# Performance work log

Hardware: AMD Instinct MI355X
Metric: run time of the kernel (lower is better)

## Reference

```python
import jax, jax.numpy as jnp
import numpy as np

# Binary (sign) weight linear: y = x @ sign(W)^T + b

def _binarize(w):
    # sign with sign(0) mapped to +1, as in typical BinaryLinear impls
    return jnp.where(w >= 0, 1.0, -1.0).astype(w.dtype)

def setup_inputs() -> dict:
    key = jax.random.key(0)
    ks = jax.random.split(key, 7)
    B = 65536
    x = jax.random.normal(ks[0], (B, 28, 28), dtype=jnp.float32)
    W1 = jax.random.normal(ks[1], (1000, 784), dtype=jnp.float32) * 0.05
    b1 = jax.random.normal(ks[2], (1000,), dtype=jnp.float32) * 0.01
    W2 = jax.random.normal(ks[3], (500, 1000), dtype=jnp.float32) * 0.05
    b2 = jax.random.normal(ks[4], (500,), dtype=jnp.float32) * 0.01
    W3 = jax.random.normal(ks[5], (10, 500), dtype=jnp.float32) * 0.05
    b3 = jax.random.normal(ks[6], (10,), dtype=jnp.float32) * 0.01
    return {"x": x, "W1": W1, "b1": b1, "W2": W2, "b2": b2, "W3": W3, "b3": b3}

def reference(x, W1, b1, W2, b2, W3, b3):
    h = x.reshape(x.shape[0], -1)                      # [B, 784]
    h = jnp.maximum(h @ _binarize(W1).T + b1, 0.0)     # [B, 1000]
    h = jnp.maximum(h @ _binarize(W2).T + b2, 0.0)     # [B, 500]
    return h @ _binarize(W3).T + b3                    # [B, 10]
```

## Files before the change

### kernel.cpp

```cpp
#include <hip/hip_runtime.h>
#include <stdint.h>


typedef __attribute__((ext_vector_type(8))) short bf16x8;
typedef __attribute__((ext_vector_type(4))) float f32x4;

typedef const __attribute__((address_space(1))) unsigned int* as1_u32p;
typedef __attribute__((address_space(3))) unsigned int* as3_u32p;

__device__ __forceinline__ void glds16(const void* g, void* l) {
  __builtin_amdgcn_global_load_lds((as1_u32p)g, (as3_u32p)l, 16, 0, 0);
}

__device__ __forceinline__ unsigned short f2bf(float f) {
  union { float f; unsigned u; } c;
  c.f = f;
  unsigned u = c.u;
  u += 0x7FFFu + ((u >> 16) & 1u);
  return (unsigned short)(u >> 16);
}

__global__ void binarize_kernel(const float* __restrict__ src, int Ns, int Ks,
                                short* __restrict__ dst, int Np, int Kp) {
  int idx = blockIdx.x * 256 + threadIdx.x;
  if (idx >= Np * Kp) return;
  int n = idx / Kp;
  int k = idx - n * Kp;
  short v = 0;
  if (n < Ns && k < Ks)
    v = (src[n * Ks + k] >= 0.0f) ? (short)0x3F80 : (short)0xBF80;
  dst[idx] = v;
}

__global__ void convert_x_kernel(const float* __restrict__ X, short* __restrict__ Xp) {
  const int g = blockIdx.x * 256 + threadIdx.x;
  if (g >= 65536 * 104) return;
  const int row = g / 104;
  const int c = (g - row * 104) * 8;
  short tmp[8];
  if (c < 784) {
    const float* s = X + (size_t)row * 784 + c;
    float4 f0 = *(const float4*)s;
    float4 f1 = *(const float4*)(s + 4);
    tmp[0] = (short)f2bf(f0.x); tmp[1] = (short)f2bf(f0.y);
    tmp[2] = (short)f2bf(f0.z); tmp[3] = (short)f2bf(f0.w);
    tmp[4] = (short)f2bf(f1.x); tmp[5] = (short)f2bf(f1.y);
    tmp[6] = (short)f2bf(f1.z); tmp[7] = (short)f2bf(f1.w);
  } else {
#pragma unroll
    for (int i = 0; i < 8; ++i) tmp[i] = 0;
  }
  *(bf16x8*)(Xp + (size_t)row * 832 + c) = *(bf16x8*)(tmp);
}

template <int KP, int NIT, int NP, int NR, int GLOG>
__global__ __launch_bounds__(256, 2)
void gemm_bk64(const short* __restrict__ A, const short* __restrict__ Wb,
               const float* __restrict__ bias, short* __restrict__ Hout) {
  __shared__ short As0[128 * 32];
  __shared__ short As1[128 * 32];
  __shared__ short Bs0[128 * 32];
  __shared__ short Bs1[128 * 32];

  const int d = blockIdx.x;
  const int xcd = d & 7;
  const int slot = d >> 3;
  const int j = slot & ((1 << GLOG) - 1);
  const int m0 = ((xcd << 6) + (slot >> GLOG)) * 128;
  const int n0 = j * 128;
  const int start = (j * NIT) >> GLOG;

  const int tid = threadIdx.x;
  const int lane = tid & 63;
  const int wave = tid >> 6;
  const int wm = wave >> 1, wn = wave & 1;
  const int l15 = lane & 15;
  const int quad = lane >> 4;

  const int sr = wave * 16 + (lane >> 2);
  const int sks = (lane & 3) * 8;
  const short* asrc = A + (size_t)(m0 + sr) * KP + sks;
  const short* bsrc = Wb + (size_t)(n0 + sr) * KP + sks;
  const int sdst = (wave * 16) * 32;

  f32x4 acc[4][4];
#pragma unroll
  for (int i = 0; i < 4; ++i)
#pragma unroll
    for (int j2 = 0; j2 < 4; ++j2) acc[i][j2] = (f32x4){0.f, 0.f, 0.f, 0.f};

  for (int it = 0; it < NIT; ++it) {
    int kit = start + it;
    if (kit >= NIT) kit -= NIT;
    const int k0 = kit * 64;

    glds16(asrc + k0, As0 + sdst);
    glds16(asrc + k0 + (size_t)64 * KP, As0 + sdst + 64 * 32);
    glds16(asrc + k0 + 32, As1 + sdst);
    glds16(asrc + k0 + 32 + (size_t)64 * KP, As1 + sdst + 64 * 32);
    glds16(bsrc + k0, Bs0 + sdst);
    glds16(bsrc + k0 + (size_t)64 * KP, Bs0 + sdst + 64 * 32);
    glds16(bsrc + k0 + 32, Bs1 + sdst);
    glds16(bsrc + k0 + 32 + (size_t)64 * KP, Bs1 + sdst + 64 * 32);
    __syncthreads();

#pragma unroll
    for (int h = 0; h < 2; ++h) {
      const short* As = h ? As1 : Bs0 - 128 * 32;
      const short* ab = (h ? As1 : As0) + (wm * 64 + l15) * 32 + quad * 8;
      const short* bb = (h ? Bs1 : Bs0) + (wn * 64 + l15) * 32 + quad * 8;
      bf16x8 af[4], bfr[4];
#pragma unroll
      for (int i = 0; i < 4; ++i) af[i] = *(const bf16x8*)(ab + i * 16 * 32);
#pragma unroll
      for (int j2 = 0; j2 < 4; ++j2) bfr[j2] = *(const bf16x8*)(bb + j2 * 16 * 32);
#pragma unroll
      for (int i = 0; i < 4; ++i)
#pragma unroll
        for (int j2 = 0; j2 < 4; ++j2)
          acc[i][j2] = __builtin_amdgcn_mfma_f32_16x16x32_bf16(af[i], bfr[j2], acc[i][j2], 0, 0, 0);
    }
    __syncthreads();
  }

#pragma unroll
  for (int j2 = 0; j2 < 4; ++j2) {
    const int n = n0 + wn * 64 + j2 * 16 + l15;
    const float bv = (n < NR) ? bias[n] : 0.f;
#pragma unroll
    for (int i = 0; i < 4; ++i) {
      const int mr = m0 + wm * 64 + i * 16 + quad * 4;
#pragma unroll
      for (int r = 0; r < 4; ++r) {
        float v = acc[i][j2][r] + bv;
        v = v > 0.f ? v : 0.f;
        Hout[(size_t)(mr + r) * NP + n] = (short)f2bf(v);
      }
    }
  }
}

__global__ __launch_bounds__(256, 2)
void gemm1_fused_kernel(const float* __restrict__ X, const short* __restrict__ Wb,
                        const float* __restrict__ bias, short* __restrict__ H) {
  constexpr int K = 784, KP = 832, NP = 1024, NR = 1000;
  __shared__ short As[128 * 32];
  __shared__ short Bs[128 * 32];

  const int tid = threadIdx.x;
  const int lane = tid & 63;
  const int wave = tid >> 6;
  const int wm = wave >> 1, wn = wave & 1;
  const int l15 = lane & 15;
  const int quad = lane >> 4;
  const int m0 = blockIdx.y * 128;
  const int n0 = blockIdx.x * 128;

  const int ar = tid >> 1;
  const int aks = (tid & 1) * 16;
  const float* xrow = X + (size_t)(m0 + ar) * K;
  short* adst = As + ar * 32 + aks;

  const int br = wave * 16 + (lane >> 2);
  const int bks = (lane & 3) * 8;
  const short* brow0 = Wb + (size_t)(n0 + br) * KP + bks;
  short* bdst = Bs + (wave * 16) * 32;

  f32x4 acc[4][4];
#pragma unroll
  for (int i = 0; i < 4; ++i)
#pragma unroll
    for (int j2 = 0; j2 < 4; ++j2) acc[i][j2] = (f32x4){0.f, 0.f, 0.f, 0.f};

  for (int k0 = 0; k0 < KP; k0 += 32) {
    glds16(brow0 + k0, bdst);
    glds16(brow0 + k0 + (size_t)64 * KP, bdst + 64 * 32);
    short tmp[16];
#pragma unroll
    for (int c = 0; c < 4; ++c) {
      const int kk = k0 + aks + c * 4;
      float4 f;
      if (kk + 3 < K)
        f = *(const float4*)(xrow + kk);
      else
        f = make_float4(0.f, 0.f, 0.f, 0.f);
      tmp[c * 4 + 0] = (short)f2bf(f.x);
      tmp[c * 4 + 1] = (short)f2bf(f.y);
      tmp[c * 4 + 2] = (short)f2bf(f.z);
      tmp[c * 4 + 3] = (short)f2bf(f.w);
    }
    *(bf16x8*)(adst) = *(bf16x8*)(tmp);
    *(bf16x8*)(adst + 8) = *(bf16x8*)(tmp + 8);
    __syncthreads();

    const short* abase = As + (size_t)(wm * 64 + l15) * 32 + quad * 8;
    const short* bbase = Bs + (size_t)(wn * 64 + l15) * 32 + quad * 8;
    bf16x8 af[4], bfr[4];
#pragma unroll
    for (int i = 0; i < 4; ++i) af[i] = *(const bf16x8*)(abase + i * 16 * 32);
#pragma unroll
    for (int j2 = 0; j2 < 4; ++j2) bfr[j2] = *(const bf16x8*)(bbase + j2 * 16 * 32);
#pragma unroll
    for (int i = 0; i < 4; ++i)
#pragma unroll
      for (int j2 = 0; j2 < 4; ++j2)
        acc[i][j2] = __builtin_amdgcn_mfma_f32_16x16x32_bf16(af[i], bfr[j2], acc[i][j2], 0, 0, 0);
    __syncthreads();
  }

#pragma unroll
  for (int j2 = 0; j2 < 4; ++j2) {
    const int n = n0 + wn * 64 + j2 * 16 + l15;
    const float bv = (n < NR) ? bias[n] : 0.f;
#pragma unroll
    for (int i = 0; i < 4; ++i) {
      const int mr = m0 + wm * 64 + i * 16 + quad * 4;
#pragma unroll
      for (int r = 0; r < 4; ++r) {
        float v = acc[i][j2][r] + bv;
        v = v > 0.f ? v : 0.f;
        H[(size_t)(mr + r) * NP + n] = (short)f2bf(v);
      }
    }
  }
}

__global__ __launch_bounds__(256, 2)
void gemm3_kernel(const short* __restrict__ Hin, const short* __restrict__ Wb,
                  const float* __restrict__ bias, float* __restrict__ Out) {
  constexpr int KP = 512;
  __shared__ short As[64 * KP];

  const int tid = threadIdx.x;
  const int lane = tid & 63;
  const int wave = tid >> 6;
  const int l15 = lane & 15;
  const int quad = lane >> 4;
  const int m0 = blockIdx.x * 64;

  bf16x8 bw[16];
#pragma unroll
  for (int kk = 0; kk < 16; ++kk)
    bw[kk] = *(const bf16x8*)(Wb + l15 * KP + kk * 32 + quad * 8);

  const short* asrc = Hin + (size_t)(m0 + wave * 16) * KP + lane * 8;
  short* adst = As + (size_t)(wave * 16) * KP;
#pragma unroll
  for (int t = 0; t < 16; ++t)
    glds16(asrc + (size_t)t * KP, adst + (size_t)t * KP);

  __syncthreads();

  f32x4 acc = (f32x4){0.f, 0.f, 0.f, 0.f};
  const short* abase = As + (size_t)(wave * 16 + l15) * KP + quad * 8;
#pragma unroll
  for (int kk = 0; kk < 16; ++kk) {
    bf16x8 af = *(const bf16x8*)(abase + kk * 32);
    acc = __builtin_amdgcn_mfma_f32_16x16x32_bf16(af, bw[kk], acc, 0, 0, 0);
  }

  if (l15 < 10) {
    const float bv = bias[l15];
#pragma unroll
    for (int r = 0; r < 4; ++r) {
      const int mr = m0 + wave * 16 + quad * 4 + r;
      Out[(size_t)mr * 10 + l15] = acc[r] + bv;
    }
  }
}

extern "C" void kernel_launch(void* const* d_in, const int* in_sizes, int n_in,
                              void* d_out, int out_size, void* d_ws, size_t ws_size,
                              hipStream_t stream) {
  const float* x = (const float*)d_in[0];
  const float* W1 = (const float*)d_in[1];
  const float* b1 = (const float*)d_in[2];
  const float* W2 = (const float*)d_in[3];
  const float* b2 = (const float*)d_in[4];
  const float* W3 = (const float*)d_in[5];
  const float* b3 = (const float*)d_in[6];
  float* out = (float*)d_out;

  const size_t szW1 = (size_t)1024 * 832 * 2;
  const size_t szW2 = (size_t)512 * 1024 * 2;
  const size_t szW3 = (size_t)16 * 512 * 2;
  const size_t szH1 = (size_t)65536 * 1024 * 2;
  const size_t szXp = (size_t)65536 * 832 * 2;
  const size_t need = szW1 + szW2 + szW3 + szH1 + szXp;

  uint8_t* p = (uint8_t*)d_ws;
  short* W1b = (short*)p; p += szW1;
  short* W2b = (short*)p; p += szW2;
  short* W3b = (short*)p; p += szW3;
  short* h1 = (short*)p; p += szH1;
  short* Z = (short*)p;

  binarize_kernel<<<(1024 * 832 + 255) / 256, 256, 0, stream>>>(W1, 1000, 784, W1b, 1024, 832);
  binarize_kernel<<<(512 * 1024 + 255) / 256, 256, 0, stream>>>(W2, 500, 1000, W2b, 512, 1024);
  binarize_kernel<<<(16 * 512 + 255) / 256, 256, 0, stream>>>(W3, 10, 500, W3b, 16, 512);

  if (ws_size >= need) {
    short* Xp = Z;
    short* h2 = Z;
    convert_x_kernel<<<(65536 * 104 + 255) / 256, 256, 0, stream>>>(x, Xp);
    gemm_bk64<832, 13, 1024, 1000, 3><<<4096, 256, 0, stream>>>(Xp, W1b, b1, h1);
    gemm_bk64<1024, 16, 512, 500, 2><<<2048, 256, 0, stream>>>(h1, W2b, b2, h2);
    gemm3_kernel<<<1024, 256, 0, stream>>>(h2, W3b, b3, out);
  } else {
    short* h2 = Z;
    gemm1_fused_kernel<<<dim3(8, 512), 256, 0, stream>>>(x, W1b, b1, h1);
    gemm_bk64<1024, 16, 512, 500, 2><<<2048, 256, 0, stream>>>(h1, W2b, b2, h2);
    gemm3_kernel<<<1024, 256, 0, stream>>>(h2, W3b, b3, out);
  }
}
```

Measured before the change: 575.2 us.

## Replace 128x128 GEMM with double-buffered 256x256 tile kernel using swizzled LDS

Replaces the 128x128, 256-thread GEMM for layers 1 and 2 with a 256x256, 512-thread kernel. The new kernel double-buffers LDS, prefetching two K-tiles ahead, and splits each K-step so that MFMA work overlaps the next global-to-LDS loads. It uses an XOR-swizzled LDS layout to avoid bank conflicts and raises wave priority around the MFMA blocks. The larger tile cuts global traffic per flop, in exchange for more LDS (128KB per block) and more accumulator registers, which may reduce occupancy.

```diff
diff --git a/kernel.cpp b/kernel.cpp
--- a/kernel.cpp
+++ b/kernel.cpp
@@ -53,86 +53,139 @@
   *(bf16x8*)(Xp + (size_t)row * 832 + c) = *(bf16x8*)(tmp);
 }
 
-template <int KP, int NIT, int NP, int NR, int GLOG>
-__global__ __launch_bounds__(256, 2)
-void gemm_bk64(const short* __restrict__ A, const short* __restrict__ Wb,
-               const float* __restrict__ bias, short* __restrict__ Hout) {
-  __shared__ short As0[128 * 32];
-  __shared__ short As1[128 * 32];
-  __shared__ short Bs0[128 * 32];
-  __shared__ short Bs1[128 * 32];
-
+template <int KP, int NKT, int NP, int NR, int NT>
+__global__ __launch_bounds__(512, 2)
+void gemm256(const short* __restrict__ A, const short* __restrict__ Wb,
+             const float* __restrict__ bias, short* __restrict__ Hout) {
+  __shared__ short Asm[2][256 * 64];
+  __shared__ short Bsm[2][256 * 64];
+
+  constexpr int NWG8 = (256 * NT) >> 3;
   const int d = blockIdx.x;
-  const int xcd = d & 7;
-  const int slot = d >> 3;
-  const int j = slot & ((1 << GLOG) - 1);
-  const int m0 = ((xcd << 6) + (slot >> GLOG)) * 128;
-  const int n0 = j * 128;
-  const int start = (j * NIT) >> GLOG;
+  const int lid = (d & 7) * NWG8 + (d >> 3);
+  const int mi = lid / NT;
+  const int ni = lid - mi * NT;
+  const int m0 = mi << 8;
+  const int n0 = ni << 8;
+  const int start = (ni * NKT) / NT;
 
   const int tid = threadIdx.x;
   const int lane = tid & 63;
-  const int wave = tid >> 6;
-  const int wm = wave >> 1, wn = wave & 1;
+  const int w = tid >> 6;
+  const int wm = w >> 2;
+  const int wn = w & 3;
   const int l15 = lane & 15;
   const int quad = lane >> 4;
 
-  const int sr = wave * 16 + (lane >> 2);
-  const int sks = (lane & 3) * 8;
-  const short* asrc = A + (size_t)(m0 + sr) * KP + sks;
-  const short* bsrc = Wb + (size_t)(n0 + sr) * KP + sks;
-  const int sdst = (wave * 16) * 32;
-
-  f32x4 acc[4][4];
-#pragma unroll
-  for (int i = 0; i < 4; ++i)
-#pragma unroll
-    for (int j2 = 0; j2 < 4; ++j2) acc[i][j2] = (f32x4){0.f, 0.f, 0.f, 0.f};
-
-  for (int it = 0; it < NIT; ++it) {
-    int kit = start + it;
-    if (kit >= NIT) kit -= NIT;
-    const int k0 = kit * 64;
-
-    glds16(asrc + k0, As0 + sdst);
-    glds16(asrc + k0 + (size_t)64 * KP, As0 + sdst + 64 * 32);
-    glds16(asrc + k0 + 32, As1 + sdst);
-    glds16(asrc + k0 + 32 + (size_t)64 * KP, As1 + sdst + 64 * 32);
-    glds16(bsrc + k0, Bs0 + sdst);
-    glds16(bsrc + k0 + (size_t)64 * KP, Bs0 + sdst + 64 * 32);
-    glds16(bsrc + k0 + 32, Bs1 + sdst);
-    glds16(bsrc + k0 + 32 + (size_t)64 * KP, Bs1 + sdst + 64 * 32);
-    __syncthreads();
-
-#pragma unroll
-    for (int h = 0; h < 2; ++h) {
-      const short* As = h ? As1 : Bs0 - 128 * 32;
-      const short* ab = (h ? As1 : As0) + (wm * 64 + l15) * 32 + quad * 8;
-      const short* bb = (h ? Bs1 : Bs0) + (wn * 64 + l15) * 32 + quad * 8;
-      bf16x8 af[4], bfr[4];
-#pragma unroll
-      for (int i = 0; i < 4; ++i) af[i] = *(const bf16x8*)(ab + i * 16 * 32);
-#pragma unroll
-      for (int j2 = 0; j2 < 4; ++j2) bfr[j2] = *(const bf16x8*)(bb + j2 * 16 * 32);
-#pragma unroll
-      for (int i = 0; i < 4; ++i)
-#pragma unroll
-        for (int j2 = 0; j2 < 4; ++j2)
-          acc[i][j2] = __builtin_amdgcn_mfma_f32_16x16x32_bf16(af[i], bfr[j2], acc[i][j2], 0, 0, 0);
-    }
-    __syncthreads();
-  }
-
-#pragma unroll
-  for (int j2 = 0; j2 < 4; ++j2) {
-    const int n = n0 + wn * 64 + j2 * 16 + l15;
+  const int srow = (w << 3) + (lane >> 3);
+  const int scol = ((lane & 7) ^ (lane >> 3)) << 3;
+  const short* ag = A + (size_t)(m0 + srow) * KP + scol;
+  const short* bg = Wb + (size_t)(n0 + srow) * KP + scol;
+  short* const la = &Asm[0][0] + (w << 9);
+  short* const lb = &Bsm[0][0] + (w << 9);
+
+  auto stageA = [&](int pb, int kit) {
+    const short* s = ag + kit * 64;
+    short* dst = la + (pb << 14);
+    glds16(s, dst);
+    glds16(s + (size_t)64 * KP, dst + 4096);
+    glds16(s + (size_t)128 * KP, dst + 8192);
+    glds16(s + (size_t)192 * KP, dst + 12288);
+  };
+  auto stageB = [&](int pb, int kit) {
+    const short* s = bg + kit * 64;
+    short* dst = lb + (pb << 14);
+    glds16(s, dst);
+    glds16(s + (size_t)64 * KP, dst + 4096);
+    glds16(s + (size_t)128 * KP, dst + 8192);
+    glds16(s + (size_t)192 * KP, dst + 12288);
+  };
+
+  const int arow = ((wm << 7) + l15) << 6;
+  const int brow = ((wn << 6) + l15) << 6;
+  const int sl0 = (quad ^ (lane & 7)) << 3;
+  const int sl1 = sl0 ^ 32;
+
+  f32x4 acc[8][4];
+#pragma unroll
+  for (int i = 0; i < 8; ++i)
+#pragma unroll
+    for (int j = 0; j < 4; ++j) acc[i][j] = (f32x4){0.f, 0.f, 0.f, 0.f};
+
+  int k1 = start + 1; if (k1 >= NKT) k1 -= NKT;
+  stageA(0, start); stageB(0, start);
+  stageA(1, k1);    stageB(1, k1);
+  asm volatile("s_waitcnt vmcnt(8)" ::: "memory");
+  __builtin_amdgcn_s_barrier();
+
+  for (int it = 0; it < NKT; ++it) {
+    const int pb = it & 1;
+    const short* Ab = &Asm[pb][0];
+    const short* Bb = &Bsm[pb][0];
+
+    bf16x8 a0[8], b0[4], a1[8], b1[4];
+#pragma unroll
+    for (int i = 0; i < 8; ++i) a0[i] = *(const bf16x8*)(Ab + arow + i * 1024 + sl0);
+#pragma unroll
+    for (int j = 0; j < 4; ++j) b0[j] = *(const bf16x8*)(Bb + brow + j * 1024 + sl0);
+    __builtin_amdgcn_s_barrier();
+    __builtin_amdgcn_s_setprio(1);
+#pragma unroll
+    for (int i = 0; i < 4; ++i)
+#pragma unroll
+      for (int j = 0; j < 4; ++j)
+        acc[i][j] = __builtin_amdgcn_mfma_f32_16x16x32_bf16(a0[i], b0[j], acc[i][j], 0, 0, 0);
+    __builtin_amdgcn_s_setprio(0);
+
+    #pragma unroll
+    for (int i = 0; i < 8; ++i) a1[i] = *(const bf16x8*)(Ab + arow + i * 1024 + sl1);
+#pragma unroll
+    for (int j = 0; j < 4; ++j) b1[j] = *(const bf16x8*)(Bb + brow + j * 1024 + sl1);
+    __builtin_amdgcn_s_barrier();
+    asm volatile("s_waitcnt lgkmcnt(0)" ::: "memory");
+    __builtin_amdgcn_s_setprio(1);
+#pragma unroll
+    for (int i = 4; i < 8; ++i)
+#pragma unroll
+      for (int j = 0; j < 4; ++j)
+        acc[i][j] = __builtin_amdgcn_mfma_f32_16x16x32_bf16(a0[i], b0[j], acc[i][j], 0, 0, 0);
+    __builtin_amdgcn_s_setprio(0);
+    __builtin_amdgcn_s_barrier();
+
+    const int it2 = it + 2;
+    int kit2 = start + it2; if (kit2 >= NKT) kit2 -= NKT;
+    const bool stg = (it2 < NKT);
+    if (stg) stageA(pb, kit2);
+    __builtin_amdgcn_s_setprio(1);
+#pragma unroll
+    for (int i = 0; i < 4; ++i)
+#pragma unroll
+      for (int j = 0; j < 4; ++j)
+        acc[i][j] = __builtin_amdgcn_mfma_f32_16x16x32_bf16(a1[i], b1[j], acc[i][j], 0, 0, 0);
+    __builtin_amdgcn_s_setprio(0);
+    if (stg) stageB(pb, kit2);
+    __builtin_amdgcn_s_setprio(1);
+#pragma unroll
+    for (int i = 4; i < 8; ++i)
+#pragma unroll
+      for (int j = 0; j < 4; ++j)
+        acc[i][j] = __builtin_amdgcn_mfma_f32_16x16x32_bf16(a1[i], b1[j], acc[i][j], 0, 0, 0);
+    __builtin_amdgcn_s_setprio(0);
+    if (stg) asm volatile("s_waitcnt vmcnt(8)" ::: "memory");
+    else     asm volatile("s_waitcnt vmcnt(0)" ::: "memory");
+    __builtin_amdgcn_s_barrier();
+  }
+
+#pragma unroll
+  for (int j = 0; j < 4; ++j) {
+    const int n = n0 + (wn << 6) + (j << 4) + l15;
     const float bv = (n < NR) ? bias[n] : 0.f;
 #pragma unroll
-    for (int i = 0; i < 4; ++i) {
-      const int mr = m0 + wm * 64 + i * 16 + quad * 4;
+    for (int i = 0; i < 8; ++i) {
+      const int mr = m0 + (wm << 7) + (i << 4) + (quad << 2);
 #pragma unroll
       for (int r = 0; r < 4; ++r) {
-        float v = acc[i][j2][r] + bv;
+        float v = acc[i][j][r] + bv;
         v = v > 0.f ? v : 0.f;
         Hout[(size_t)(mr + r) * NP + n] = (short)f2bf(v);
       }
@@ -303,13 +356,13 @@
     short* Xp = Z;
     short* h2 = Z;
     convert_x_kernel<<<(65536 * 104 + 255) / 256, 256, 0, stream>>>(x, Xp);
-    gemm_bk64<832, 13, 1024, 1000, 3><<<4096, 256, 0, stream>>>(Xp, W1b, b1, h1);
-    gemm_bk64<1024, 16, 512, 500, 2><<<2048, 256, 0, stream>>>(h1, W2b, b2, h2);
+    gemm256<832, 13, 1024, 1000, 4><<<1024, 512, 0, stream>>>(Xp, W1b, b1, h1);
+    gemm256<1024, 16, 512, 500, 2><<<512, 512, 0, stream>>>(h1, W2b, b2, h2);
     gemm3_kernel<<<1024, 256, 0, stream>>>(h2, W3b, b3, out);
   } else {
     short* h2 = Z;
     gemm1_fused_kernel<<<dim3(8, 512), 256, 0, stream>>>(x, W1b, b1, h1);
-    gemm_bk64<1024, 16, 512, 500, 2><<<2048, 256, 0, stream>>>(h1, W2b, b2, h2);
+    gemm256<1024, 16, 512, 500, 2><<<512, 512, 0, stream>>>(h1, W2b, b2, h2);
     gemm3_kernel<<<1024, 256, 0, stream>>>(h2, W3b, b3, out);
   }
 }
```

After: 581.4 us. Within noise of the previous version (+1.1%).
